# Kernel tuning notes

Measured on AMD Instinct MI355X. Metric: run time of the kernel, lower is better.

Reference implementation:

```python
import jax, jax.numpy as jnp
import numpy as np

ALPHA = 10.0  # anchor scale: anchors = eye(C) * ALPHA


def setup_inputs() -> dict:
    key = jax.random.key(0)
    k_x, k_w = jax.random.split(key)
    B, D, C = 16384, 768, 1024
    x = jax.random.normal(k_x, (B, D), dtype=jnp.float32)
    # nn.Linear(input_dim, num_classes, bias=False).weight has shape (C, D)
    W = jax.random.normal(k_w, (C, D), dtype=jnp.float32) * (1.0 / np.sqrt(D))
    return {"x": x, "W": W}


def reference(x, W):
    # logits: (B, C) = x @ W^T
    logits = jnp.einsum("bd,cd->bc", x, W)
    # distances[b, j] = || logits[b] - alpha * e_j ||_2
    # = sqrt(||logits[b]||^2 - 2*alpha*logits[b, j] + alpha^2)
    # (exact algebraic identity for diagonal anchors; avoids the (B, C, C) intermediate)
    sq_norm = jnp.sum(logits * logits, axis=-1, keepdims=True)  # (B, 1)
    d2 = sq_norm - 2.0 * ALPHA * logits + ALPHA * ALPHA          # (B, C)
    distances = jnp.sqrt(jnp.maximum(d2, 0.0))
    return logits, distances
```

## Files before the change

kernel.cpp:

```cpp
#include <hip/hip_runtime.h>
#include <hip/hip_bf16.h>
#include <stdint.h>


#define M_DIM 16384
#define N_DIM 1024
#define K_DIM 768
#define ALPHA_F 10.0f

typedef __bf16 bf16x8 __attribute__((ext_vector_type(8)));
typedef float f32x4 __attribute__((ext_vector_type(4)));

static __device__ __forceinline__ bf16x8 cvt8(f32x4 a, f32x4 b) {
  union { __bf16 h[8]; bf16x8 v; } p;
  p.h[0] = (__bf16)a[0]; p.h[1] = (__bf16)a[1];
  p.h[2] = (__bf16)a[2]; p.h[3] = (__bf16)a[3];
  p.h[4] = (__bf16)b[0]; p.h[5] = (__bf16)b[1];
  p.h[6] = (__bf16)b[2]; p.h[7] = (__bf16)b[3];
  return p.v;
}

__global__ __launch_bounds__(256) void cvt_w_kernel(const float* __restrict__ Wm,
                                                    unsigned short* __restrict__ Wq) {
  int tid = blockIdx.x * 256 + threadIdx.x;
  int l15 = tid & 15;
  int q = (tid >> 4) & 3;
  int mi = (tid >> 6) & 7;
  int rem = tid >> 9;
  int kt = rem % 24;
  int chunk = rem / 24;
  int col = chunk * 128 + mi * 16 + l15;
  int k = kt * 32 + q * 8;
  const f32x4* p = (const f32x4*)(Wm + (size_t)col * K_DIM + k);
  *(bf16x8*)(Wq + (size_t)tid * 8) = cvt8(p[0], p[1]);
}

__global__ __launch_bounds__(512, 4) void fused_kernel(
    const float* __restrict__ X,
    const unsigned short* __restrict__ Wq,
    float* __restrict__ logits,
    float* __restrict__ dist) {
  __shared__ __align__(16) unsigned short xt[32 * 768];
  __shared__ float rs[32][8];

  const int t = threadIdx.x;
  const int lane = t & 63;
  const int w = t >> 6;
  const int q = lane >> 4;
  const int l15 = lane & 15;

  const int bid = blockIdx.x;
  const int tm = (bid & 7) * 64 + (bid >> 3);

  const float* Xb = X + (size_t)tm * 32 * K_DIM;

#pragma unroll
  for (int r = 0; r < 6; ++r) {
    int id = r * 512 + t;
    int row = id / 96;
    int c = id - row * 96;
    const f32x4* g = (const f32x4*)(Xb + (size_t)row * K_DIM + c * 8);
    f32x4 a = g[0], b = g[1];
    *(bf16x8*)(&xt[row * 768 + (c ^ (row & 7)) * 8]) = cvt8(a, b);
  }
  __syncthreads();

  f32x4 acc[8][2] = {};
  const unsigned short* wchunk = Wq + ((size_t)(w * 24) * 512 + lane) * 8;
#pragma unroll 2
  for (int kt = 0; kt < 24; ++kt) {
    bf16x8 bx[2];
#pragma unroll
    for (int ni = 0; ni < 2; ++ni) {
      int row = ni * 16 + l15;
      bx[ni] = *(const bf16x8*)(&xt[row * 768 + ((kt * 4 + q) ^ (row & 7)) * 8]);
    }
    const unsigned short* wp = wchunk + (size_t)kt * 512 * 8;
    bf16x8 af[8];
#pragma unroll
    for (int mi = 0; mi < 8; ++mi) af[mi] = *(const bf16x8*)(wp + mi * 512);
#pragma unroll
    for (int mi = 0; mi < 8; ++mi)
#pragma unroll
      for (int ni = 0; ni < 2; ++ni)
        acc[mi][ni] = __builtin_amdgcn_mfma_f32_16x16x32_bf16(af[mi], bx[ni], acc[mi][ni], 0, 0, 0);
  }

  float part[2];
#pragma unroll
  for (int ni = 0; ni < 2; ++ni) {
    float s = 0.f;
#pragma unroll
    for (int mi = 0; mi < 8; ++mi)
#pragma unroll
      for (int j = 0; j < 4; ++j) { float v = acc[mi][ni][j]; s += v * v; }
    part[ni] = s;
  }
#pragma unroll
  for (int m = 16; m <= 32; m <<= 1)
#pragma unroll
    for (int ni = 0; ni < 2; ++ni) part[ni] += __shfl_xor(part[ni], m, 64);
  if (q == 0) {
#pragma unroll
    for (int ni = 0; ni < 2; ++ni) rs[ni * 16 + l15][w] = part[ni];
  }
  __syncthreads();

  float S[2];
#pragma unroll
  for (int ni = 0; ni < 2; ++ni) {
    const float* rp = &rs[ni * 16 + l15][0];
    f32x4 a = *(const f32x4*)(rp + 0);
    f32x4 b = *(const f32x4*)(rp + 4);
    S[ni] = (a[0] + a[1] + a[2] + a[3]) + (b[0] + b[1] + b[2] + b[3]);
  }

  const float a2 = ALPHA_F * ALPHA_F;
  float* Lb = logits + (size_t)tm * 32 * N_DIM + w * 128 + q * 4;
  float* Db = dist + (size_t)tm * 32 * N_DIM + w * 128 + q * 4;
#pragma unroll
  for (int ni = 0; ni < 2; ++ni) {
    size_t roff = (size_t)(ni * 16 + l15) * N_DIM;
#pragma unroll
    for (int mi = 0; mi < 8; ++mi) {
      f32x4 lv = acc[mi][ni];
      *(f32x4*)(Lb + roff + mi * 16) = lv;
      f32x4 d;
#pragma unroll
      for (int j = 0; j < 4; ++j)
        d[j] = sqrtf(fmaxf(S[ni] - 2.0f * ALPHA_F * lv[j] + a2, 0.0f));
      *(f32x4*)(Db + roff + mi * 16) = d;
    }
  }
}

extern "C" void kernel_launch(void* const* d_in, const int* in_sizes, int n_in,
                              void* d_out, int out_size, void* d_ws, size_t ws_size,
                              hipStream_t stream) {
  const float* x = (const float*)d_in[0];
  const float* W = (const float*)d_in[1];
  float* logits = (float*)d_out;
  float* dist = logits + (size_t)M_DIM * N_DIM;

  unsigned short* Wq = (unsigned short*)d_ws;

  cvt_w_kernel<<<(N_DIM * K_DIM / 8) / 256, 256, 0, stream>>>(W, Wq);
  fused_kernel<<<M_DIM / 32, 512, 0, stream>>>(x, Wq, logits, dist);
}
```

Baseline: 68.13 us.

## Use 1024-thread blocks processing two row tiles with prefetched X

Doubles the block to 16 waves, so each wave owns 64 output columns instead of 128, which halves the accumulator registers per wave. Each block now walks two 32-row tiles in turn. The second tile's X rows are loaded into registers during the first tile's reduction and epilogue, then converted into shared memory, overlapping global loads with compute. In exchange, half as many blocks launch, there are extra barriers, and 1024-thread blocks with launch_bounds(1024,4) may limit occupancy.

```diff
diff --git a/kernel.cpp b/kernel.cpp
--- a/kernel.cpp
+++ b/kernel.cpp
@@ -35,13 +35,13 @@
   *(bf16x8*)(Wq + (size_t)tid * 8) = cvt8(p[0], p[1]);
 }
 
-__global__ __launch_bounds__(512, 4) void fused_kernel(
+__global__ __launch_bounds__(1024, 4) void fused_kernel(
     const float* __restrict__ X,
     const unsigned short* __restrict__ Wq,
     float* __restrict__ logits,
     float* __restrict__ dist) {
   __shared__ __align__(16) unsigned short xt[32 * 768];
-  __shared__ float rs[32][8];
+  __shared__ float rs[32][16];
 
   const int t = threadIdx.x;
   const int lane = t & 63;
@@ -50,87 +50,127 @@
   const int l15 = lane & 15;
 
   const int bid = blockIdx.x;
-  const int tm = (bid & 7) * 64 + (bid >> 3);
+  const int tm = (bid & 7) * 32 + (bid >> 3);
 
-  const float* Xb = X + (size_t)tm * 32 * K_DIM;
+  const unsigned short* wchunk =
+      Wq + ((size_t)((w >> 1) * 24) * 512 + (w & 1) * 256 + lane) * 8;
+  const float a2 = ALPHA_F * ALPHA_F;
 
+  int srow[3], sc[3];
 #pragma unroll
-  for (int r = 0; r < 6; ++r) {
-    int id = r * 512 + t;
-    int row = id / 96;
-    int c = id - row * 96;
-    const f32x4* g = (const f32x4*)(Xb + (size_t)row * K_DIM + c * 8);
-    f32x4 a = g[0], b = g[1];
-    *(bf16x8*)(&xt[row * 768 + (c ^ (row & 7)) * 8]) = cvt8(a, b);
+  for (int j = 0; j < 3; ++j) {
+    int id = j * 1024 + t;
+    srow[j] = id / 96;
+    sc[j] = id - srow[j] * 96;
+  }
+
+  f32x4 acc[4][2];
+  f32x4 hr[6];
+
+  {
+    const float* Xb = X + (size_t)tm * 64 * K_DIM;
+#pragma unroll
+    for (int j = 0; j < 3; ++j) {
+      const f32x4* g = (const f32x4*)(Xb + (size_t)srow[j] * K_DIM + sc[j] * 8);
+      f32x4 a = g[0], b = g[1];
+      *(bf16x8*)(&xt[srow[j] * 768 + (sc[j] ^ (srow[j] & 7)) * 8]) = cvt8(a, b);
+    }
   }
   __syncthreads();
 
-  f32x4 acc[8][2] = {};
-  const unsigned short* wchunk = Wq + ((size_t)(w * 24) * 512 + lane) * 8;
+#pragma unroll
+  for (int tile = 0; tile < 2; ++tile) {
+    const int rowbase = tm * 64 + tile * 32;
+#pragma unroll
+    for (int mi = 0; mi < 4; ++mi)
+#pragma unroll
+      for (int ni = 0; ni < 2; ++ni) acc[mi][ni] = (f32x4)0.f;
+
 #pragma unroll 2
-  for (int kt = 0; kt < 24; ++kt) {
-    bf16x8 bx[2];
+    for (int kt = 0; kt < 24; ++kt) {
+      bf16x8 bx[2];
+#pragma unroll
+      for (int ni = 0; ni < 2; ++ni) {
+        int row = ni * 16 + l15;
+        bx[ni] = *(const bf16x8*)(&xt[row * 768 + ((kt * 4 + q) ^ (row & 7)) * 8]);
+      }
+      const unsigned short* wp = wchunk + (size_t)kt * 512 * 8;
+#pragma unroll
+      for (int mi = 0; mi < 4; ++mi) {
+        bf16x8 af = *(const bf16x8*)(wp + mi * 512);
+#pragma unroll
+        for (int ni = 0; ni < 2; ++ni)
+          acc[mi][ni] = __builtin_amdgcn_mfma_f32_16x16x32_bf16(af, bx[ni], acc[mi][ni], 0, 0, 0);
+      }
+    }
+
+    if (tile == 0) {
+      const float* Xb = X + (size_t)(tm * 64 + 32) * K_DIM;
+#pragma unroll
+      for (int j = 0; j < 3; ++j) {
+        const f32x4* g = (const f32x4*)(Xb + (size_t)srow[j] * K_DIM + sc[j] * 8);
+        hr[2 * j] = g[0];
+        hr[2 * j + 1] = g[1];
+      }
+    }
+
+    float part[2];
 #pragma unroll
     for (int ni = 0; ni < 2; ++ni) {
-      int row = ni * 16 + l15;
-      bx[ni] = *(const bf16x8*)(&xt[row * 768 + ((kt * 4 + q) ^ (row & 7)) * 8]);
+      float s = 0.f;
+#pragma unroll
+      for (int mi = 0; mi < 4; ++mi)
+#pragma unroll
+        for (int j = 0; j < 4; ++j) { float v = acc[mi][ni][j]; s += v * v; }
+      part[ni] = s;
     }
-    const unsigned short* wp = wchunk + (size_t)kt * 512 * 8;
-    bf16x8 af[8];
 #pragma unroll
-    for (int mi = 0; mi < 8; ++mi) af[mi] = *(const bf16x8*)(wp + mi * 512);
+    for (int m = 16; m <= 32; m <<= 1)
 #pragma unroll
-    for (int mi = 0; mi < 8; ++mi)
+      for (int ni = 0; ni < 2; ++ni) part[ni] += __shfl_xor(part[ni], m, 64);
+    if (q == 0) {
 #pragma unroll
-      for (int ni = 0; ni < 2; ++ni)
-        acc[mi][ni] = __builtin_amdgcn_mfma_f32_16x16x32_bf16(af[mi], bx[ni], acc[mi][ni], 0, 0, 0);
-  }
+      for (int ni = 0; ni < 2; ++ni) rs[ni * 16 + l15][w] = part[ni];
+    }
+    __syncthreads();
 
-  float part[2];
+    float S[2];
 #pragma unroll
-  for (int ni = 0; ni < 2; ++ni) {
-    float s = 0.f;
+    for (int ni = 0; ni < 2; ++ni) {
+      const float* rp = &rs[ni * 16 + l15][0];
+      f32x4 a = *(const f32x4*)(rp + 0);
+      f32x4 b = *(const f32x4*)(rp + 4);
+      f32x4 c = *(const f32x4*)(rp + 8);
+      f32x4 d = *(const f32x4*)(rp + 12);
+      S[ni] = ((a[0] + a[1] + a[2] + a[3]) + (b[0] + b[1] + b[2] + b[3])) +
+              ((c[0] + c[1] + c[2] + c[3]) + (d[0] + d[1] + d[2] + d[3]));
+    }
+
+    if (tile == 0) {
 #pragma unroll
-    for (int mi = 0; mi < 8; ++mi)
+      for (int j = 0; j < 3; ++j)
+        *(bf16x8*)(&xt[srow[j] * 768 + (sc[j] ^ (srow[j] & 7)) * 8]) =
+            cvt8(hr[2 * j], hr[2 * j + 1]);
+    }
+
+    float* Lb = logits + (size_t)rowbase * N_DIM + w * 64 + q * 4;
+    float* Db = dist + (size_t)rowbase * N_DIM + w * 64 + q * 4;
 #pragma unroll
-      for (int j = 0; j < 4; ++j) { float v = acc[mi][ni][j]; s += v * v; }
-    part[ni] = s;
-  }
+    for (int ni = 0; ni < 2; ++ni) {
+      size_t roff = (size_t)(ni * 16 + l15) * N_DIM;
 #pragma unroll
-  for (int m = 16; m <= 32; m <<= 1)
+      for (int mi = 0; mi < 4; ++mi) {
+        f32x4 lv = acc[mi][ni];
+        *(f32x4*)(Lb + roff + mi * 16) = lv;
+        f32x4 d;
 #pragma unroll
-    for (int ni = 0; ni < 2; ++ni) part[ni] += __shfl_xor(part[ni], m, 64);
-  if (q == 0) {
-#pragma unroll
-    for (int ni = 0; ni < 2; ++ni) rs[ni * 16 + l15][w] = part[ni];
-  }
-  __syncthreads();
+        for (int j = 0; j < 4; ++j)
+          d[j] = sqrtf(fmaxf(S[ni] - 2.0f * ALPHA_F * lv[j] + a2, 0.0f));
+        *(f32x4*)(Db + roff + mi * 16) = d;
+      }
+    }
 
-  float S[2];
-#pragma unroll
-  for (int ni = 0; ni < 2; ++ni) {
-    const float* rp = &rs[ni * 16 + l15][0];
-    f32x4 a = *(const f32x4*)(rp + 0);
-    f32x4 b = *(const f32x4*)(rp + 4);
-    S[ni] = (a[0] + a[1] + a[2] + a[3]) + (b[0] + b[1] + b[2] + b[3]);
-  }
-
-  const float a2 = ALPHA_F * ALPHA_F;
-  float* Lb = logits + (size_t)tm * 32 * N_DIM + w * 128 + q * 4;
-  float* Db = dist + (size_t)tm * 32 * N_DIM + w * 128 + q * 4;
-#pragma unroll
-  for (int ni = 0; ni < 2; ++ni) {
-    size_t roff = (size_t)(ni * 16 + l15) * N_DIM;
-#pragma unroll
-    for (int mi = 0; mi < 8; ++mi) {
-      f32x4 lv = acc[mi][ni];
-      *(f32x4*)(Lb + roff + mi * 16) = lv;
-      f32x4 d;
-#pragma unroll
-      for (int j = 0; j < 4; ++j)
-        d[j] = sqrtf(fmaxf(S[ni] - 2.0f * ALPHA_F * lv[j] + a2, 0.0f));
-      *(f32x4*)(Db + roff + mi * 16) = d;
-    }
+    if (tile == 0) __syncthreads();
   }
 }
 
@@ -145,5 +185,5 @@
   unsigned short* Wq = (unsigned short*)d_ws;
 
   cvt_w_kernel<<<(N_DIM * K_DIM / 8) / 256, 256, 0, stream>>>(W, Wq);
-  fused_kernel<<<M_DIM / 32, 512, 0, stream>>>(x, Wq, logits, dist);
+  fused_kernel<<<M_DIM / 64, 1024, 0, stream>>>(x, Wq, logits, dist);
 }
```

After: 70.22 us. 1.03x slower.
